# Kernel optimization log

Hardware: AMD Instinct MI355X
Metric: run time of the kernel (lower is better)

The kernel has to match this reference:

```python
import jax, jax.numpy as jnp
import numpy as np

EPS = 1e-7  # K.epsilon()
NUM_ROUTING = 3


def squash(v, axis=-1):
    s2 = jnp.sum(jnp.square(v), axis=axis, keepdims=True)
    scale = s2 / (1.0 + s2) / jnp.sqrt(s2 + EPS)
    return scale * v


def setup_inputs() -> dict:
    key = jax.random.key(0)
    k1, k2 = jax.random.split(key)
    B, IN_CAPS, IN_DIM = 64, 4096, 8
    N_CAPS, DIM = 16, 16
    inputs = jax.random.normal(k1, (B, IN_CAPS, IN_DIM), dtype=jnp.float32)
    W = jax.random.normal(k2, (N_CAPS, IN_CAPS, DIM, IN_DIM), dtype=jnp.float32) * 0.05
    return {"inputs": inputs, "W": W}


def reference(inputs, W):
    # u_hat[b,j,i,d] = sum_e W[j,i,d,e] * inputs[b,i,e]
    inputs_hat = jnp.einsum('bie,jide->bjid', inputs, W)  # [B, nc, inum, dim]
    b = jnp.zeros(inputs_hat.shape[:3], dtype=inputs_hat.dtype)  # [B, nc, inum]
    outputs = None
    for i in range(NUM_ROUTING):
        c = jax.nn.softmax(b, axis=1)  # softmax over output capsules (dim=1 in source)
        s = jnp.einsum('bji,bjid->bjd', c, inputs_hat)  # weighted combine
        outputs = squash(s)  # [B, nc, dim]
        if i < NUM_ROUTING - 1:
            b = b + jnp.einsum('bjd,bjid->bji', outputs, inputs_hat)  # agreement
    return outputs
```

## Files before the change

kernel.cpp:

```cpp
#include <hip/hip_runtime.h>
#include <math.h>

#define B_   64
#define IC_  4096
#define NC_  16
#define D_   16
#define IPB  16
#define CH_  2
#define WROW 68
#define XROW 68

typedef __fp16 half2v __attribute__((ext_vector_type(2)));

#if __has_builtin(__builtin_amdgcn_fdot2)
#define HAVE_FDOT2 1
#else
#define HAVE_FDOT2 0
#endif

__device__ inline unsigned pk16(float a, float b) {
    half2v h = __builtin_amdgcn_cvt_pkrtz(a, b);
    return __builtin_bit_cast(unsigned, h);
}

__device__ inline float hdot2(unsigned w, unsigned x, float cacc) {
#if HAVE_FDOT2
    return __builtin_amdgcn_fdot2(__builtin_bit_cast(half2v, w),
                                  __builtin_bit_cast(half2v, x), cacc, false);
#else
    half2v hw = __builtin_bit_cast(half2v, w);
    half2v hx = __builtin_bit_cast(half2v, x);
    return cacc + (float)hw.x * (float)hx.x + (float)hw.y * (float)hx.y;
#endif
}

template <int CTRL>
__device__ inline float ror_add(float v) {
    int r = __builtin_amdgcn_update_dpp(0, __float_as_int(v), CTRL, 0xf, 0xf, false);
    return v + __int_as_float(r);
}

__global__ __launch_bounds__(512, 4)
void caps_pass(const float* __restrict__ inp, const float* __restrict__ W,
               const float* __restrict__ osum, unsigned* __restrict__ partials,
               int use_osum)
{
    __shared__ unsigned wlds[2][CH_ * NC_ * WROW];
    __shared__ unsigned xlds[32 * XROW];

    const int tid = threadIdx.x;
    const int j   = tid & 15;
    const int c   = (tid >> 4) & 3;
    const int wv  = tid >> 6;

    const int n   = blockIdx.x;
    const int cpx = gridDim.x >> 3;
    const int wg  = (n & 7) * cpx + (n >> 3);
    const int ib  = wg >> 1;
    const int bg  = wg & 1;
    const int i0  = ib * IPB;
    const int b0  = bg * 32 + wv * 4;

    {
        const int xb = tid >> 4, xil = tid & 15;
        const float4* src =
            (const float4*)inp + ((size_t)(bg * 32 + xb) * IC_ + i0 + xil) * 2;
        float4 xa = src[0], xbv = src[1];
        *(uint4*)&xlds[xb * XROW + xil * 4] =
            make_uint4(pk16(xa.x, xa.y), pk16(xa.z, xa.w),
                       pk16(xbv.x, xbv.y), pk16(xbv.z, xbv.w));
    }

    const int srow = tid >> 4;
    const int scol = tid & 15;
    const int sil  = srow >> 4;
    const int sj   = srow & 15;
    const float4* Wf4 = (const float4*)W;
    const size_t wgbase = ((size_t)sj * IC_) * 32 + scol * 2;

    float4 g0, g1;
    g0 = Wf4[wgbase + (size_t)(i0 + sil) * 32];
    g1 = Wf4[wgbase + (size_t)(i0 + sil) * 32 + 1];
    *(uint4*)&wlds[0][srow * WROW + scol * 4] =
        make_uint4(pk16(g0.x, g0.y), pk16(g0.z, g0.w),
                   pk16(g1.x, g1.y), pk16(g1.z, g1.w));
    __syncthreads();

    float4 os[4];
    if (use_osum) {
#pragma unroll
        for (int bi = 0; bi < 4; ++bi) {
            float4 o = ((const float4*)osum)[((size_t)(b0 + bi) * 16 + j) * 4 + c];
            const float L2E = 1.44269504f;
            os[bi] = make_float4(o.x * L2E, o.y * L2E, o.z * L2E, o.w * L2E);
        }
    }

    float acc[4][4];
#pragma unroll
    for (int bi = 0; bi < 4; ++bi)
#pragma unroll
        for (int dl = 0; dl < 4; ++dl) acc[bi][dl] = 0.0f;

    const int nch = IPB / CH_;
    int cur = 0;
    for (int ch = 0; ch < nch; ++ch) {
        if (ch + 1 < nch) {
            const int inx = i0 + (ch + 1) * CH_ + sil;
            g0 = Wf4[wgbase + (size_t)inx * 32];
            g1 = Wf4[wgbase + (size_t)inx * 32 + 1];
        }
#pragma unroll
        for (int il = 0; il < CH_; ++il) {
            const int ilg = ch * CH_ + il;
            const unsigned* wr = &wlds[cur][(il * NC_ + j) * WROW + c * 16];
            uint4 q0 = *(const uint4*)&wr[0];
            uint4 q1 = *(const uint4*)&wr[4];
            uint4 q2 = *(const uint4*)&wr[8];
            uint4 q3 = *(const uint4*)&wr[12];

            uint4 xh[4];
#pragma unroll
            for (int bi = 0; bi < 4; ++bi)
                xh[bi] = *(const uint4*)&xlds[(wv * 4 + bi) * XROW + ilg * 4];

            float uh[4][4];
#pragma unroll
            for (int dl = 0; dl < 4; ++dl) {
                uint4 qq = (dl == 0) ? q0 : (dl == 1) ? q1 : (dl == 2) ? q2 : q3;
#pragma unroll
                for (int bi = 0; bi < 4; ++bi) {
                    float r = hdot2(qq.x, xh[bi].x, 0.0f);
                    r = hdot2(qq.y, xh[bi].y, r);
                    r = hdot2(qq.z, xh[bi].z, r);
                    uh[bi][dl] = hdot2(qq.w, xh[bi].w, r);
                }
            }

            float cc[4];
            if (use_osum) {
                float pb[4];
#pragma unroll
                for (int bi = 0; bi < 4; ++bi) {
                    float t = os[bi].x * uh[bi][0];
                    t = fmaf(os[bi].y, uh[bi][1], t);
                    t = fmaf(os[bi].z, uh[bi][2], t);
                    t = fmaf(os[bi].w, uh[bi][3], t);
                    pb[bi] = t;
                }
#pragma unroll
                for (int bi = 0; bi < 4; ++bi) {
                    pb[bi] += __shfl_xor(pb[bi], 16);
                    pb[bi] += __shfl_xor(pb[bi], 32);
                }
#pragma unroll
                for (int bi = 0; bi < 4; ++bi) {
                    float e  = exp2f(pb[bi]);
                    float sm = ror_add<0x128>(e);
                    sm = ror_add<0x124>(sm);
                    sm = ror_add<0x122>(sm);
                    sm = ror_add<0x121>(sm);
                    cc[bi] = __fdividef(e, sm);
                }
            } else {
#pragma unroll
                for (int bi = 0; bi < 4; ++bi) cc[bi] = 0.0625f;
            }

#pragma unroll
            for (int bi = 0; bi < 4; ++bi)
#pragma unroll
                for (int dl = 0; dl < 4; ++dl)
                    acc[bi][dl] = fmaf(cc[bi], uh[bi][dl], acc[bi][dl]);
        }
        if (ch + 1 < nch) {
            const int nb = cur ^ 1;
            *(uint4*)&wlds[nb][srow * WROW + scol * 4] =
                make_uint4(pk16(g0.x, g0.y), pk16(g0.z, g0.w),
                           pk16(g1.x, g1.y), pk16(g1.z, g1.w));
        }
        __syncthreads();
        cur ^= 1;
    }

#pragma unroll
    for (int bi = 0; bi < 4; ++bi) {
        unsigned lo = pk16(acc[bi][0], acc[bi][1]);
        unsigned hi = pk16(acc[bi][2], acc[bi][3]);
        *(uint2*)&partials[(size_t)ib * (B_ * NC_ * 8) +
                           ((size_t)(b0 + bi) * NC_ + j) * 8 + c * 2] =
            make_uint2(lo, hi);
    }
}

__global__ __launch_bounds__(256)
void caps_reduce(const unsigned* __restrict__ partials, float* __restrict__ osum,
                 float* __restrict__ outb, int NI, int mode)
{
    __shared__ float4 red[256];
    const int tid = threadIdx.x;
    const int q   = tid & 3;
    const int ks  = tid >> 2;
    const int bj  = blockIdx.x;

    float4 s = make_float4(0.f, 0.f, 0.f, 0.f);
    for (int ibk = ks; ibk < NI; ibk += 64) {
        uint2 v = *(const uint2*)&partials[(size_t)ibk * (B_ * NC_ * 8) +
                                           (size_t)bj * 8 + q * 2];
        half2v h0 = __builtin_bit_cast(half2v, v.x);
        half2v h1 = __builtin_bit_cast(half2v, v.y);
        s.x += (float)h0.x; s.y += (float)h0.y;
        s.z += (float)h1.x; s.w += (float)h1.y;
    }
    red[tid] = s;
    __syncthreads();
    if (tid < 64) {
        float4 a = red[tid], b = red[tid + 64], cc = red[tid + 128], d = red[tid + 192];
        s.x = a.x + b.x + cc.x + d.x; s.y = a.y + b.y + cc.y + d.y;
        s.z = a.z + b.z + cc.z + d.z; s.w = a.w + b.w + cc.w + d.w;
        red[tid] = s;
    }
    __syncthreads();
    if (tid < 4) {
        float4 t = red[tid];
#pragma unroll
        for (int kk = 1; kk < 16; ++kk) {
            float4 v = red[kk * 4 + tid];
            t.x += v.x; t.y += v.y; t.z += v.z; t.w += v.w;
        }
        float s2 = t.x * t.x + t.y * t.y + t.z * t.z + t.w * t.w;
        s2 += __shfl_xor(s2, 1);
        s2 += __shfl_xor(s2, 2);
        float scale = s2 / (1.0f + s2) * rsqrtf(s2 + 1e-7f);
        float4 o = make_float4(scale * t.x, scale * t.y, scale * t.z, scale * t.w);
        size_t fi = (size_t)bj * 4 + tid;
        if (mode == 0) ((float4*)osum)[fi] = o;
        else if (mode == 1) {
            float4 cu = ((float4*)osum)[fi];
            cu.x += o.x; cu.y += o.y; cu.z += o.z; cu.w += o.w;
            ((float4*)osum)[fi] = cu;
        } else ((float4*)outb)[fi] = o;
    }
}

extern "C" void kernel_launch(void* const* d_in, const int* in_sizes, int n_in,
                              void* d_out, int out_size, void* d_ws, size_t ws_size,
                              hipStream_t stream)
{
    const float* inp = (const float*)d_in[0];
    const float* W   = (const float*)d_in[1];
    float* out  = (float*)d_out;

    float*    osum     = (float*)d_ws;
    unsigned* partials = (unsigned*)((char*)d_ws + 65536);

    const int NI = IC_ / IPB;
    dim3 grid(2 * NI);

    caps_pass<<<grid, 512, 0, stream>>>(inp, W, osum, partials, 0);
    caps_reduce<<<1024, 256, 0, stream>>>(partials, osum, out, NI, 0);
    caps_pass<<<grid, 512, 0, stream>>>(inp, W, osum, partials, 1);
    caps_reduce<<<1024, 256, 0, stream>>>(partials, osum, out, NI, 1);
    caps_pass<<<grid, 512, 0, stream>>>(inp, W, osum, partials, 1);
    caps_reduce<<<1024, 256, 0, stream>>>(partials, osum, out, NI, 2);
}
```

Measured before the change: 114.7 us.

## Compute u_hat with MFMA 16x16x32 f16 and restructure per-block tiling

Replaces the scalar fdot2-based u_hat computation with MFMA 16x16x32 f16 instructions. Each block now covers 8 input capsules across all 64 batches instead of 16 capsules by 32 batches. W is staged in an MFMA-friendly LDS layout, and two wave halves over input capsules are combined through LDS before writing partials. In routing passes u_hat is computed twice per capsule (once for agreement, once for the weighted sum), and the 16x32 K dimension is half-zero-padded for lanes >=16. This trades redundant matrix work for matrix-core throughput and drops the double-buffered W pipeline.

After: 163.2 us. +42.4%, slower.

```diff
diff --git a/kernel.cpp b/kernel.cpp
--- a/kernel.cpp
+++ b/kernel.cpp
@@ -5,191 +5,181 @@
 #define IC_  4096
 #define NC_  16
 #define D_   16
-#define IPB  16
-#define CH_  2
-#define WROW 68
-#define XROW 68
-
+#define IPB  8
+#define XROW 34
+
+typedef __fp16 half8  __attribute__((ext_vector_type(8)));
 typedef __fp16 half2v __attribute__((ext_vector_type(2)));
-
-#if __has_builtin(__builtin_amdgcn_fdot2)
-#define HAVE_FDOT2 1
-#else
-#define HAVE_FDOT2 0
-#endif
+typedef float  f32x4  __attribute__((ext_vector_type(4)));
 
 __device__ inline unsigned pk16(float a, float b) {
     half2v h = __builtin_amdgcn_cvt_pkrtz(a, b);
     return __builtin_bit_cast(unsigned, h);
 }
-
-__device__ inline float hdot2(unsigned w, unsigned x, float cacc) {
-#if HAVE_FDOT2
+__device__ inline float hdot2(unsigned w, unsigned x, float c) {
     return __builtin_amdgcn_fdot2(__builtin_bit_cast(half2v, w),
-                                  __builtin_bit_cast(half2v, x), cacc, false);
-#else
-    half2v hw = __builtin_bit_cast(half2v, w);
-    half2v hx = __builtin_bit_cast(half2v, x);
-    return cacc + (float)hw.x * (float)hx.x + (float)hw.y * (float)hx.y;
-#endif
-}
-
-template <int CTRL>
-__device__ inline float ror_add(float v) {
-    int r = __builtin_amdgcn_update_dpp(0, __float_as_int(v), CTRL, 0xf, 0xf, false);
-    return v + __int_as_float(r);
-}
-
-__global__ __launch_bounds__(512, 4)
+                                  __builtin_bit_cast(half2v, x), c, false);
+}
+__device__ inline half8 h8(uint4 v) { return __builtin_bit_cast(half8, v); }
+
+__global__ __launch_bounds__(512)
 void caps_pass(const float* __restrict__ inp, const float* __restrict__ W,
                const float* __restrict__ osum, unsigned* __restrict__ partials,
                int use_osum)
 {
-    __shared__ unsigned wlds[2][CH_ * NC_ * WROW];
-    __shared__ unsigned xlds[32 * XROW];
-
-    const int tid = threadIdx.x;
-    const int j   = tid & 15;
-    const int c   = (tid >> 4) & 3;
-    const int wv  = tid >> 6;
+    __shared__ unsigned wlds[8192];
+    __shared__ unsigned xlds[64 * XROW];
+
+    const int tid   = threadIdx.x;
+    const int lane  = tid & 63;
+    const int l15   = lane & 15;
+    const int g     = lane >> 4;
+    const int wv    = tid >> 6;
+    const int btile = wv & 3;
+    const int ihalf = wv >> 2;
 
     const int n   = blockIdx.x;
     const int cpx = gridDim.x >> 3;
-    const int wg  = (n & 7) * cpx + (n >> 3);
-    const int ib  = wg >> 1;
-    const int bg  = wg & 1;
+    const int ib  = (n & 7) * cpx + (n >> 3);
     const int i0  = ib * IPB;
-    const int b0  = bg * 32 + wv * 4;
 
     {
-        const int xb = tid >> 4, xil = tid & 15;
-        const float4* src =
-            (const float4*)inp + ((size_t)(bg * 32 + xb) * IC_ + i0 + xil) * 2;
-        float4 xa = src[0], xbv = src[1];
-        *(uint4*)&xlds[xb * XROW + xil * 4] =
-            make_uint4(pk16(xa.x, xa.y), pk16(xa.z, xa.w),
-                       pk16(xbv.x, xbv.y), pk16(xbv.z, xbv.w));
-    }
-
-    const int srow = tid >> 4;
-    const int scol = tid & 15;
-    const int sil  = srow >> 4;
-    const int sj   = srow & 15;
-    const float4* Wf4 = (const float4*)W;
-    const size_t wgbase = ((size_t)sj * IC_) * 32 + scol * 2;
-
-    float4 g0, g1;
-    g0 = Wf4[wgbase + (size_t)(i0 + sil) * 32];
-    g1 = Wf4[wgbase + (size_t)(i0 + sil) * 32 + 1];
-    *(uint4*)&wlds[0][srow * WROW + scol * 4] =
-        make_uint4(pk16(g0.x, g0.y), pk16(g0.z, g0.w),
-                   pk16(g1.x, g1.y), pk16(g1.z, g1.w));
-    __syncthreads();
-
-    float4 os[4];
-    if (use_osum) {
-#pragma unroll
-        for (int bi = 0; bi < 4; ++bi) {
-            float4 o = ((const float4*)osum)[((size_t)(b0 + bi) * 16 + j) * 4 + c];
-            const float L2E = 1.44269504f;
-            os[bi] = make_float4(o.x * L2E, o.y * L2E, o.z * L2E, o.w * L2E);
-        }
-    }
-
-    float acc[4][4];
-#pragma unroll
-    for (int bi = 0; bi < 4; ++bi)
-#pragma unroll
-        for (int dl = 0; dl < 4; ++dl) acc[bi][dl] = 0.0f;
-
-    const int nch = IPB / CH_;
-    int cur = 0;
-    for (int ch = 0; ch < nch; ++ch) {
-        if (ch + 1 < nch) {
-            const int inx = i0 + (ch + 1) * CH_ + sil;
-            g0 = Wf4[wgbase + (size_t)inx * 32];
-            g1 = Wf4[wgbase + (size_t)inx * 32 + 1];
-        }
-#pragma unroll
-        for (int il = 0; il < CH_; ++il) {
-            const int ilg = ch * CH_ + il;
-            const unsigned* wr = &wlds[cur][(il * NC_ + j) * WROW + c * 16];
-            uint4 q0 = *(const uint4*)&wr[0];
-            uint4 q1 = *(const uint4*)&wr[4];
-            uint4 q2 = *(const uint4*)&wr[8];
-            uint4 q3 = *(const uint4*)&wr[12];
-
-            uint4 xh[4];
-#pragma unroll
-            for (int bi = 0; bi < 4; ++bi)
-                xh[bi] = *(const uint4*)&xlds[(wv * 4 + bi) * XROW + ilg * 4];
-
-            float uh[4][4];
-#pragma unroll
-            for (int dl = 0; dl < 4; ++dl) {
-                uint4 qq = (dl == 0) ? q0 : (dl == 1) ? q1 : (dl == 2) ? q2 : q3;
-#pragma unroll
-                for (int bi = 0; bi < 4; ++bi) {
-                    float r = hdot2(qq.x, xh[bi].x, 0.0f);
-                    r = hdot2(qq.y, xh[bi].y, r);
-                    r = hdot2(qq.z, xh[bi].z, r);
-                    uh[bi][dl] = hdot2(qq.w, xh[bi].w, r);
+        const int xb = tid >> 3, io = tid & 7;
+        const float4* src = (const float4*)inp + ((size_t)xb * IC_ + i0 + io) * 2;
+        float4 a = src[0], b = src[1];
+        *(uint4*)&xlds[xb * XROW + io * 4] =
+            make_uint4(pk16(a.x, a.y), pk16(a.z, a.w), pk16(b.x, b.y), pk16(b.z, b.w));
+    }
+    {
+        const float4* Wf4 = (const float4*)W;
+#pragma unroll
+        for (int it = 0; it < 4; ++it) {
+            int u  = it * 512 + tid;
+            int il = u >> 8, j = (u >> 4) & 15, d = u & 15;
+            size_t gidx = (((size_t)j * IC_ + i0 + il) * 16 + d) * 2;
+            float4 a = Wf4[gidx], b = Wf4[gidx + 1];
+            int widx = ((il * 4 + (j >> 2)) * 4 + (d >> 2)) * 64 + ((j & 3) * 4 + (d & 3)) * 4;
+            *(uint4*)&wlds[widx] =
+                make_uint4(pk16(a.x, a.y), pk16(a.z, a.w), pk16(b.x, b.y), pk16(b.z, b.w));
+        }
+    }
+    __syncthreads();
+
+    const int b16 = btile * 16 + l15;
+    const f32x4 zero4 = {0.f, 0.f, 0.f, 0.f};
+
+    f32x4 acc[4][4];
+#pragma unroll
+    for (int a1 = 0; a1 < 4; ++a1)
+#pragma unroll
+        for (int a2 = 0; a2 < 4; ++a2) acc[a1][a2] = zero4;
+
+    if (!use_osum) {
+        const int ilb = ihalf * 4;
+        uint4 xf = *(const uint4*)&xlds[b16 * XROW + (ilb + g) * 4];
+        half8 xb8 = h8(xf);
+#pragma unroll
+        for (int jq = 0; jq < 4; ++jq)
+#pragma unroll
+            for (int q = 0; q < 4; ++q) {
+                uint4 wf = *(const uint4*)&wlds[(((ilb + g) * 4 + jq) * 4 + q) * 64 + l15 * 4];
+                acc[jq][q] = __builtin_amdgcn_mfma_f32_16x16x32_f16(
+                    h8(wf), xb8, acc[jq][q], 0, 0, 0);
+            }
+    } else {
+        unsigned osh[4][8];
+        const float L2E = 1.44269504f;
+#pragma unroll
+        for (int jq = 0; jq < 4; ++jq) {
+            const float4* op = (const float4*)osum + ((size_t)b16 * 16 + 4 * jq + g) * 4;
+#pragma unroll
+            for (int q = 0; q < 4; ++q) {
+                float4 o = op[q];
+                osh[jq][q * 2]     = pk16(o.x * L2E, o.y * L2E);
+                osh[jq][q * 2 + 1] = pk16(o.z * L2E, o.w * L2E);
+            }
+        }
+        const bool lo = lane < 16;
+#pragma unroll
+        for (int ii = 0; ii < 4; ++ii) {
+            const int il = ihalf * 4 + ii;
+            uint4 xf = make_uint4(0, 0, 0, 0);
+            if (lo) xf = *(const uint4*)&xlds[b16 * XROW + il * 4];
+            half8 xb8 = h8(xf);
+
+            float pb0 = 0.f, pb1 = 0.f, pb2 = 0.f, pb3 = 0.f;
+#pragma unroll
+            for (int jq = 0; jq < 4; ++jq) {
+#pragma unroll
+                for (int q = 0; q < 4; ++q) {
+                    uint4 wf = make_uint4(0, 0, 0, 0);
+                    if (lo) wf = *(const uint4*)&wlds[((il * 4 + jq) * 4 + q) * 64 + l15 * 4];
+                    f32x4 C = __builtin_amdgcn_mfma_f32_16x16x32_f16(
+                        h8(wf), xb8, zero4, 0, 0, 0);
+                    unsigned p0 = pk16(C[0], C[1]);
+                    unsigned p1 = pk16(C[2], C[3]);
+                    float t = hdot2(osh[jq][q * 2], p0, 0.f);
+                    t = hdot2(osh[jq][q * 2 + 1], p1, t);
+                    if (jq == 0) pb0 += t; else if (jq == 1) pb1 += t;
+                    else if (jq == 2) pb2 += t; else pb3 += t;
                 }
             }
-
-            float cc[4];
-            if (use_osum) {
-                float pb[4];
-#pragma unroll
-                for (int bi = 0; bi < 4; ++bi) {
-                    float t = os[bi].x * uh[bi][0];
-                    t = fmaf(os[bi].y, uh[bi][1], t);
-                    t = fmaf(os[bi].z, uh[bi][2], t);
-                    t = fmaf(os[bi].w, uh[bi][3], t);
-                    pb[bi] = t;
+            float e0 = exp2f(pb0), e1 = exp2f(pb1), e2 = exp2f(pb2), e3 = exp2f(pb3);
+            float den = (e0 + e1) + (e2 + e3);
+            den += __shfl_xor(den, 16);
+            den += __shfl_xor(den, 32);
+            float r = __fdividef(1.f, den);
+            float cc0 = e0 * r, cc1 = e1 * r, cc2 = e2 * r, cc3 = e3 * r;
+
+#pragma unroll
+            for (int jq = 0; jq < 4; ++jq) {
+                float ccj = (jq == 0) ? cc0 : (jq == 1) ? cc1 : (jq == 2) ? cc2 : cc3;
+#pragma unroll
+                for (int q = 0; q < 4; ++q) {
+                    uint4 wf = make_uint4(0, 0, 0, 0);
+                    if (lo) wf = *(const uint4*)&wlds[((il * 4 + jq) * 4 + q) * 64 + l15 * 4];
+                    f32x4 C = __builtin_amdgcn_mfma_f32_16x16x32_f16(
+                        h8(wf), xb8, zero4, 0, 0, 0);
+                    acc[jq][q][0] = fmaf(ccj, C[0], acc[jq][q][0]);
+                    acc[jq][q][1] = fmaf(ccj, C[1], acc[jq][q][1]);
+                    acc[jq][q][2] = fmaf(ccj, C[2], acc[jq][q][2]);
+                    acc[jq][q][3] = fmaf(ccj, C[3], acc[jq][q][3]);
                 }
-#pragma unroll
-                for (int bi = 0; bi < 4; ++bi) {
-                    pb[bi] += __shfl_xor(pb[bi], 16);
-                    pb[bi] += __shfl_xor(pb[bi], 32);
-                }
-#pragma unroll
-                for (int bi = 0; bi < 4; ++bi) {
-                    float e  = exp2f(pb[bi]);
-                    float sm = ror_add<0x128>(e);
-                    sm = ror_add<0x124>(sm);
-                    sm = ror_add<0x122>(sm);
-                    sm = ror_add<0x121>(sm);
-                    cc[bi] = __fdividef(e, sm);
-                }
-            } else {
-#pragma unroll
-                for (int bi = 0; bi < 4; ++bi) cc[bi] = 0.0625f;
-            }
-
-#pragma unroll
-            for (int bi = 0; bi < 4; ++bi)
-#pragma unroll
-                for (int dl = 0; dl < 4; ++dl)
-                    acc[bi][dl] = fmaf(cc[bi], uh[bi][dl], acc[bi][dl]);
-        }
-        if (ch + 1 < nch) {
-            const int nb = cur ^ 1;
-            *(uint4*)&wlds[nb][srow * WROW + scol * 4] =
-                make_uint4(pk16(g0.x, g0.y), pk16(g0.z, g0.w),
-                           pk16(g1.x, g1.y), pk16(g1.z, g1.w));
-        }
-        __syncthreads();
-        cur ^= 1;
-    }
-
-#pragma unroll
-    for (int bi = 0; bi < 4; ++bi) {
-        unsigned lo = pk16(acc[bi][0], acc[bi][1]);
-        unsigned hi = pk16(acc[bi][2], acc[bi][3]);
-        *(uint2*)&partials[(size_t)ib * (B_ * NC_ * 8) +
-                           ((size_t)(b0 + bi) * NC_ + j) * 8 + c * 2] =
-            make_uint2(lo, hi);
+            }
+        }
+    }
+
+    __syncthreads();
+    if (ihalf == 1) {
+        unsigned* dst = &wlds[(btile * 64 + lane) * 32];
+#pragma unroll
+        for (int jq = 0; jq < 4; ++jq)
+#pragma unroll
+            for (int q = 0; q < 4; ++q) {
+                dst[(jq * 4 + q) * 2]     = pk16(acc[jq][q][0], acc[jq][q][1]);
+                dst[(jq * 4 + q) * 2 + 1] = pk16(acc[jq][q][2], acc[jq][q][3]);
+            }
+    }
+    __syncthreads();
+    if (ihalf == 0) {
+        const unsigned* srcp = &wlds[(btile * 64 + lane) * 32];
+        const float sc = use_osum ? 1.0f : 0.0625f;
+#pragma unroll
+        for (int jq = 0; jq < 4; ++jq) {
+            const int j = 4 * jq + g;
+#pragma unroll
+            for (int q = 0; q < 4; ++q) {
+                half2v ha = __builtin_bit_cast(half2v, srcp[(jq * 4 + q) * 2]);
+                half2v hb = __builtin_bit_cast(half2v, srcp[(jq * 4 + q) * 2 + 1]);
+                float s0 = (acc[jq][q][0] + (float)ha.x) * sc;
+                float s1 = (acc[jq][q][1] + (float)ha.y) * sc;
+                float s2 = (acc[jq][q][2] + (float)hb.x) * sc;
+                float s3 = (acc[jq][q][3] + (float)hb.y) * sc;
+                *(uint2*)&partials[(size_t)ib * (B_ * NC_ * 8) +
+                                   ((size_t)b16 * 16 + j) * 8 + q * 2] =
+                    make_uint2(pk16(s0, s1), pk16(s2, s3));
+            }
+        }
     }
 }
 
@@ -255,7 +245,7 @@
     unsigned* partials = (unsigned*)((char*)d_ws + 65536);
 
     const int NI = IC_ / IPB;
-    dim3 grid(2 * NI);
+    dim3 grid(NI);
 
     caps_pass<<<grid, 512, 0, stream>>>(inp, W, osum, partials, 0);
     caps_reduce<<<1024, 256, 0, stream>>>(partials, osum, out, NI, 0);
```

## Use MFMA matrix cores for first routing pass with uniform coupling

Applied to the files above, without the earlier changes.

Adds a dedicated first-iteration kernel for the routing pass. Because the coupling coefficients are uniform (1/16) in that pass, the weighted sum over input capsules folds into a K dimension. The kernel computes it with 16x16x32 f16 MFMA instructions in place of the generic fdot2 path, writing fp16 partials scaled by 1/16 in the layout the reduce kernel expects. It launches half as many blocks as the generic pass. The risk is that the partials layout no longer matches what caps_reduce expects, and the fp16 accumulation order changes.

Result: faster. 109.4 us (-4.6%).

```diff
diff --git a/kernel.cpp b/kernel.cpp
--- a/kernel.cpp
+++ b/kernel.cpp
@@ -10,7 +10,9 @@
 #define WROW 68
 #define XROW 68
 
+typedef __fp16 half8  __attribute__((ext_vector_type(8)));
 typedef __fp16 half2v __attribute__((ext_vector_type(2)));
+typedef float  f32x4  __attribute__((ext_vector_type(4)));
 
 #if __has_builtin(__builtin_amdgcn_fdot2)
 #define HAVE_FDOT2 1
@@ -22,7 +24,6 @@
     half2v h = __builtin_amdgcn_cvt_pkrtz(a, b);
     return __builtin_bit_cast(unsigned, h);
 }
-
 __device__ inline float hdot2(unsigned w, unsigned x, float cacc) {
 #if HAVE_FDOT2
     return __builtin_amdgcn_fdot2(__builtin_bit_cast(half2v, w),
@@ -33,11 +34,87 @@
     return cacc + (float)hw.x * (float)hx.x + (float)hw.y * (float)hx.y;
 #endif
 }
+__device__ inline half8 h8(uint4 v) { return __builtin_bit_cast(half8, v); }
 
 template <int CTRL>
 __device__ inline float ror_add(float v) {
     int r = __builtin_amdgcn_update_dpp(0, __float_as_int(v), CTRL, 0xf, 0xf, false);
     return v + __int_as_float(r);
+}
+
+__global__ __launch_bounds__(512)
+void caps_pass0(const float* __restrict__ inp, const float* __restrict__ W,
+                unsigned* __restrict__ partials)
+{
+    __shared__ unsigned xlds[64 * XROW];
+
+    const int tid  = threadIdx.x;
+    const int lane = tid & 63;
+    const int l15  = lane & 15;
+    const int g    = lane >> 4;
+    const int wv   = tid >> 6;
+
+    const int n   = blockIdx.x;
+    const int cpx = gridDim.x >> 3;
+    const int ib  = (n & 7) * cpx + (n >> 3);
+    const int i0  = ib * IPB;
+
+    {
+        const int xb = tid >> 3;
+        const int io = (tid & 7) * 2;
+#pragma unroll
+        for (int r = 0; r < 2; ++r) {
+            const float4* src =
+                (const float4*)inp + ((size_t)xb * IC_ + i0 + io + r) * 2;
+            float4 a = src[0], b = src[1];
+            *(uint4*)&xlds[xb * XROW + (io + r) * 4] =
+                make_uint4(pk16(a.x, a.y), pk16(a.z, a.w),
+                           pk16(b.x, b.y), pk16(b.z, b.w));
+        }
+    }
+    __syncthreads();
+
+    const int j0 = wv * 2;
+    f32x4 acc[2][4];
+#pragma unroll
+    for (int jj = 0; jj < 2; ++jj)
+#pragma unroll
+        for (int bt = 0; bt < 4; ++bt) acc[jj][bt] = (f32x4){0.f, 0.f, 0.f, 0.f};
+
+#pragma unroll
+    for (int kc = 0; kc < 4; ++kc) {
+        half8 afrag[2];
+#pragma unroll
+        for (int jj = 0; jj < 2; ++jj) {
+            const float4* wp = (const float4*)W +
+                (((size_t)(j0 + jj) * IC_ + i0 + kc * 4 + g) * 16 + l15) * 2;
+            float4 a = wp[0], b = wp[1];
+            afrag[jj] = h8(make_uint4(pk16(a.x, a.y), pk16(a.z, a.w),
+                                      pk16(b.x, b.y), pk16(b.z, b.w)));
+        }
+#pragma unroll
+        for (int bt = 0; bt < 4; ++bt) {
+            uint4 xf = *(const uint4*)&xlds[(bt * 16 + l15) * XROW + (kc * 4 + g) * 4];
+            half8 bfrag = h8(xf);
+#pragma unroll
+            for (int jj = 0; jj < 2; ++jj)
+                acc[jj][bt] = __builtin_amdgcn_mfma_f32_16x16x32_f16(
+                    afrag[jj], bfrag, acc[jj][bt], 0, 0, 0);
+        }
+    }
+
+#pragma unroll
+    for (int jj = 0; jj < 2; ++jj)
+#pragma unroll
+        for (int bt = 0; bt < 4; ++bt) {
+            f32x4 C = acc[jj][bt];
+            unsigned lo = pk16(C[0] * 0.0625f, C[1] * 0.0625f);
+            unsigned hi = pk16(C[2] * 0.0625f, C[3] * 0.0625f);
+            size_t b = bt * 16 + l15;
+            *(uint2*)&partials[(size_t)ib * (B_ * NC_ * 8) +
+                               (b * 16 + (j0 + jj)) * 8 + g * 2] =
+                make_uint2(lo, hi);
+        }
 }
 
 __global__ __launch_bounds__(512, 4)
@@ -257,7 +334,7 @@
     const int NI = IC_ / IPB;
     dim3 grid(2 * NI);
 
-    caps_pass<<<grid, 512, 0, stream>>>(inp, W, osum, partials, 0);
+    caps_pass0<<<NI, 512, 0, stream>>>(inp, W, partials);
     caps_reduce<<<1024, 256, 0, stream>>>(partials, osum, out, NI, 0);
     caps_pass<<<grid, 512, 0, stream>>>(inp, W, osum, partials, 1);
     caps_reduce<<<1024, 256, 0, stream>>>(partials, osum, out, NI, 1);
```
